# Kernel optimization log

Measured on AMD Instinct MI355X. Metric: run time of the kernel, lower is better.

Reference implementation:

```python
import jax, jax.numpy as jnp
import numpy as np

PATCH = 8
EPS = 1e-5


def _conv2d(x, w, b, groups=1, padding='VALID'):
    # x: NCHW, w: OIHW
    y = jax.lax.conv_general_dilated(
        x, w, window_strides=(1, 1), padding=padding,
        feature_group_count=groups,
        dimension_numbers=('NCHW', 'OIHW', 'NCHW'))
    return y + b[None, :, None, None]


def setup_inputs() -> dict:
    key = jax.random.key(0)
    ks = jax.random.split(key, 8)
    B, C, H, W = 4, 48, 256, 256
    C6, C2 = C * 6, C * 2
    x = jax.random.normal(ks[0], (B, C, H, W), dtype=jnp.float32)
    w_hidden = jax.random.normal(ks[1], (C6, C, 1, 1), dtype=jnp.float32) * 0.05
    b_hidden = jnp.zeros((C6,), dtype=jnp.float32)
    w_dw = jax.random.normal(ks[2], (C6, 1, 3, 3), dtype=jnp.float32) * 0.05
    b_dw = jnp.zeros((C6,), dtype=jnp.float32)
    gamma = jnp.ones((C2,), dtype=jnp.float32)
    beta = jnp.zeros((C2,), dtype=jnp.float32)
    w_out = jax.random.normal(ks[3], (C, C2, 1, 1), dtype=jnp.float32) * 0.05
    b_out = jnp.zeros((C,), dtype=jnp.float32)
    return {'x': x, 'w_hidden': w_hidden, 'b_hidden': b_hidden,
            'w_dw': w_dw, 'b_dw': b_dw, 'gamma': gamma, 'beta': beta,
            'w_out': w_out, 'b_out': b_out}


def reference(x, w_hidden, b_hidden, w_dw, b_dw, gamma, beta, w_out, b_out):
    B, C, H, W = x.shape
    C6 = 6 * C
    hidden = _conv2d(x, w_hidden, b_hidden)                       # [B,6C,H,W]
    qkv = _conv2d(hidden, w_dw, b_dw, groups=C6, padding='SAME')  # depthwise 3x3
    q, k, v = jnp.split(qkv, 3, axis=1)                           # each [B,2C,H,W]
    C2 = 2 * C
    hp, wp = H // PATCH, W // PATCH
    # same flat reshape as torch .reshape(b,c,h/p,w/p,p,p)
    q_patch = q.reshape(B, C2, hp, wp, PATCH, PATCH)
    k_patch = k.reshape(B, C2, hp, wp, PATCH, PATCH)
    q_fft = jnp.fft.rfft2(q_patch)                                # complex, last two axes
    k_fft = jnp.fft.rfft2(k_patch)
    out = jnp.fft.irfft2(q_fft * k_fft, s=(PATCH, PATCH))
    out = out.reshape(B, C2, H, W)
    # LayerNorm over channel dim (torch LayerNorm(2C) on [B,HW,2C])
    mu = jnp.mean(out, axis=1, keepdims=True)
    var = jnp.var(out, axis=1, keepdims=True)
    normed = (out - mu) / jnp.sqrt(var + EPS)
    normed = normed * gamma[None, :, None, None] + beta[None, :, None, None]
    return _conv2d(v * normed, w_out, b_out)                      # [B,C,H,W]
```

## Files before the change

### kernel.cpp

```cpp
#include <hip/hip_runtime.h>


#define B_ 4
#define C_ 48
#define H_ 256
#define W_ 256
#define ROWS 68
#define XT_STR 52
#define HID_STR 204
#define QK_STR 68
#define AV_STR 40

#define OFF_HID 0
#define OFF_QS  6528
#define OFF_KS  10880
#define OFF_OSH 15232
#define OFF_MU  27520
#define OFF_RS  27776
#define SMEM_BYTES 28032

typedef __attribute__((ext_vector_type(8))) short short8;
typedef __attribute__((ext_vector_type(4))) float floatx4;
union U128 { unsigned long long u[2]; short8 s; };

__device__ __forceinline__ float bf2f(unsigned short u) {
  return __uint_as_float(((unsigned int)u) << 16);
}
__device__ __forceinline__ unsigned short f2bf(float f) {
  unsigned int x = __float_as_uint(f);
  x += 0x7FFFu + ((x >> 16) & 1u);
  return (unsigned short)(x >> 16);
}
__device__ __forceinline__ unsigned long long pack4(float a, float b, float c, float d) {
  return (unsigned long long)f2bf(a) | ((unsigned long long)f2bf(b) << 16) |
         ((unsigned long long)f2bf(c) << 32) | ((unsigned long long)f2bf(d) << 48);
}

__global__ void fsas_prep(const float* __restrict__ wh, const float* __restrict__ wo,
                          unsigned short* __restrict__ ws) {
  int idx = blockIdx.x * 256 + threadIdx.x;
  if (idx < 12288) {
    int kk = idx & 63, t = idx >> 6;
    int m = t & 31, ch = t >> 5;
    float v = 0.f;
    if (kk < 48) {
      int c6 = (m < 16) ? (ch * 16 + m) : (96 + ch * 16 + (m - 16));
      v = wh[c6 * 48 + kk];
    }
    ws[idx] = f2bf(v);
  } else if (idx < 18432) {
    int e = idx - 12288;
    int kk = e & 63, t = e >> 6;
    int m = t & 15, ch = t >> 4;
    float v = (kk < 48) ? wh[(192 + ch * 16 + m) * 48 + kk] : 0.f;
    ws[idx] = f2bf(v);
  } else if (idx < 23040) {
    int e = idx - 18432;
    int kk = e & 31, t = e >> 5;
    int co = t % 48, pr = t / 48;
    ws[idx] = f2bf(wo[co * 96 + pr * 32 + kk]);
  }
}

__global__ __launch_bounds__(256, 4) void fsas_fused(
    const float* __restrict__ x,   const float* __restrict__ bh,
    const float* __restrict__ wdw, const float* __restrict__ bdw,
    const float* __restrict__ gam, const float* __restrict__ bet,
    const float* __restrict__ bo,  const unsigned short* __restrict__ ws,
    float* __restrict__ y)
{
  __shared__ __align__(16) char smem[SMEM_BYTES];
  unsigned short* xs_t = (unsigned short*)(smem);
  unsigned short* hid  = (unsigned short*)(smem + OFF_HID);
  float* qs = (float*)(smem + OFF_QS);
  float* ks = (float*)(smem + OFF_KS);
  unsigned short* osh = (unsigned short*)(smem + OFF_OSH);
  float* mu = (float*)(smem + OFF_MU);
  float* rs = (float*)(smem + OFF_RS);
  unsigned short* avp = (unsigned short*)(smem + OFF_QS);
  float2* part = (float2*)(smem + OFF_HID);

  const unsigned short* wqk = ws;
  const unsigned short* wv1 = ws + 12288;
  const unsigned short* w2p = ws + 18432;

  const int tid  = threadIdx.x;
  const int wseg = blockIdx.x;
  const int h    = blockIdx.y;
  const int b    = blockIdx.z;
  const int w0   = wseg * 64;
  const int lane = tid & 63;
  const int wv   = tid >> 6;
  const int ln   = lane & 15;
  const int quad = lane >> 4;
  const int pbase = wv * 16 + ln;

  for (int p = tid; p < 208; p += 256)
    *(unsigned long long*)(xs_t + p * XT_STR + 48) = 0ull;
  if (tid < 8) *(unsigned int*)(smem + 21632 + tid * 4) = 0u;
  for (int r = wv; r < 144; r += 4) {
    int c = r / 3, rr = r - c * 3;
    int gr = h - 1 + rr;
    bool rok = (gr >= 0) && (gr < H_);
    const float* xrow = x + (((b * C_) + c) * H_ + (rok ? gr : 0)) * W_;
    {
      int cc = lane, gc = w0 - 1 + cc;
      float v = 0.f;
      if (rok && gc >= 0 && gc < W_) v = xrow[gc];
      xs_t[(rr * ROWS + cc) * XT_STR + c] = f2bf(v);
    }
    if (lane < 4) {
      int cc = 64 + lane, gc = w0 - 1 + cc;
      float v = 0.f;
      if (cc < 66 && rok && gc < W_) v = xrow[gc];
      xs_t[(rr * ROWS + cc) * XT_STR + c] = f2bf(v);
    }
  }
  __syncthreads();

  short8 f00, f01, f10, f11, f20, f21, f30, f31;
  int pvm = 0;
  {
    U128 t0, t1;
    const unsigned short* bp0 = xs_t + (pbase)       * XT_STR + quad * 8;
    const unsigned short* bp1 = xs_t + (pbase + 64)  * XT_STR + quad * 8;
    const unsigned short* bp2 = xs_t + (pbase + 128) * XT_STR + quad * 8;
    t0.u[0] = *(const unsigned long long*)(bp0);
    t0.u[1] = *(const unsigned long long*)(bp0 + 4);
    t1.u[0] = *(const unsigned long long*)(bp0 + 32);
    t1.u[1] = *(const unsigned long long*)(bp0 + 36);
    asm("" : "=a"(f00) : "0"(t0.s));
    asm("" : "=a"(f01) : "0"(t1.s));
    t0.u[0] = *(const unsigned long long*)(bp1);
    t0.u[1] = *(const unsigned long long*)(bp1 + 4);
    t1.u[0] = *(const unsigned long long*)(bp1 + 32);
    t1.u[1] = *(const unsigned long long*)(bp1 + 36);
    asm("" : "=a"(f10) : "0"(t0.s));
    asm("" : "=a"(f11) : "0"(t1.s));
    t0.u[0] = *(const unsigned long long*)(bp2);
    t0.u[1] = *(const unsigned long long*)(bp2 + 4);
    t1.u[0] = *(const unsigned long long*)(bp2 + 32);
    t1.u[1] = *(const unsigned long long*)(bp2 + 36);
    asm("" : "=a"(f20) : "0"(t0.s));
    asm("" : "=a"(f21) : "0"(t1.s));
    t0.u[0] = 0ull; t0.u[1] = 0ull; t1.u[0] = 0ull; t1.u[1] = 0ull;
    if (wv == 0) {
      const unsigned short* bp3 = xs_t + (pbase + 192) * XT_STR + quad * 8;
      t0.u[0] = *(const unsigned long long*)(bp3);
      t0.u[1] = *(const unsigned long long*)(bp3 + 4);
      t1.u[0] = *(const unsigned long long*)(bp3 + 32);
      t1.u[1] = *(const unsigned long long*)(bp3 + 36);
    }
    asm("" : "=a"(f30) : "0"(t0.s));
    asm("" : "=a"(f31) : "0"(t1.s));
    #pragma unroll
    for (int i = 0; i < 4; ++i) {
      int p = pbase + i * 64;
      int rr = p / ROWS, cc = p - rr * ROWS;
      int gr = h - 1 + rr, gc = w0 - 1 + cc;
      bool pv = (rr < 3) && (cc < 66) && (gr >= 0) && (gr < H_) && (gc >= 0) && (gc < W_);
      pvm |= (pv ? 1 : 0) << i;
    }
  }
  __syncthreads();

  auto run_b1 = [&](const unsigned short* wA, int arow, int bhb) {
    short8 a0 = *(const short8*)(wA + ((arow + ln) * 64 + quad * 8));
    short8 a1 = *(const short8*)(wA + ((arow + ln) * 64 + 32 + quad * 8));
    floatx4 bb;
    #pragma unroll
    for (int r = 0; r < 4; ++r) bb[r] = bh[bhb + quad * 4 + r];
    unsigned short* hb = hid + (quad * 4) * HID_STR + pbase;
    {
      floatx4 acc = bb;
      acc = __builtin_amdgcn_mfma_f32_16x16x32_bf16(a0, f00, acc, 0, 0, 0);
      acc = __builtin_amdgcn_mfma_f32_16x16x32_bf16(a1, f01, acc, 0, 0, 0);
      bool pv = (pvm & 1) != 0;
      #pragma unroll
      for (int r = 0; r < 4; ++r) hb[r * HID_STR] = pv ? f2bf(acc[r]) : (unsigned short)0;
    }
    {
      floatx4 acc = bb;
      acc = __builtin_amdgcn_mfma_f32_16x16x32_bf16(a0, f10, acc, 0, 0, 0);
      acc = __builtin_amdgcn_mfma_f32_16x16x32_bf16(a1, f11, acc, 0, 0, 0);
      bool pv = (pvm & 2) != 0;
      #pragma unroll
      for (int r = 0; r < 4; ++r) hb[r * HID_STR + 64] = pv ? f2bf(acc[r]) : (unsigned short)0;
    }
    {
      floatx4 acc = bb;
      acc = __builtin_amdgcn_mfma_f32_16x16x32_bf16(a0, f20, acc, 0, 0, 0);
      acc = __builtin_amdgcn_mfma_f32_16x16x32_bf16(a1, f21, acc, 0, 0, 0);
      bool pv = (pvm & 4) != 0;
      #pragma unroll
      for (int r = 0; r < 4; ++r) hb[r * HID_STR + 128] = pv ? f2bf(acc[r]) : (unsigned short)0;
    }
    if (wv == 0) {
      floatx4 acc = bb;
      acc = __builtin_amdgcn_mfma_f32_16x16x32_bf16(a0, f30, acc, 0, 0, 0);
      acc = __builtin_amdgcn_mfma_f32_16x16x32_bf16(a1, f31, acc, 0, 0, 0);
      bool pv = (pvm & 8) != 0;
      if (ln < 12) {
        #pragma unroll
        for (int r = 0; r < 4; ++r) hb[r * HID_STR + 192] = pv ? f2bf(acc[r]) : (unsigned short)0;
      }
    }
  };
  auto run_b2 = [&](int c6base, float* dst) {
    int cl = tid >> 4, pg4 = tid & 15, p0 = pg4 * 4;
    int c6 = c6base + cl;
    const float* wd = wdw + c6 * 9;
    float bb = bdw[c6];
    float a4[4] = {bb, bb, bb, bb};
    #pragma unroll
    for (int di = 0; di < 3; ++di) {
      const unsigned short* hrow = hid + cl * HID_STR + di * ROWS + p0;
      unsigned long long lo = *(const unsigned long long*)(hrow);
      unsigned int ex = *(const unsigned int*)(hrow + 4);
      float hf[6];
      #pragma unroll
      for (int t = 0; t < 4; ++t) hf[t] = bf2f((unsigned short)(lo >> (16 * t)));
      hf[4] = bf2f((unsigned short)ex);
      hf[5] = bf2f((unsigned short)(ex >> 16));
      #pragma unroll
      for (int dj = 0; dj < 3; ++dj) {
        float w = wd[di * 3 + dj];
        #pragma unroll
        for (int t = 0; t < 4; ++t) a4[t] += w * hf[t + dj];
      }
    }
    *(float4*)(dst + cl * QK_STR + p0) = make_float4(a4[0], a4[1], a4[2], a4[3]);
  };
  auto run_b3 = [&](int c2base) {
    int cl = tid >> 4, r4 = tid & 15, uu = r4 >> 1, vh = r4 & 1;
    const float* qrow = qs + cl * QK_STR;
    const float* krow = ks + cl * QK_STR;
    float a4[4] = {0.f, 0.f, 0.f, 0.f};
    #pragma unroll
    for (int i = 0; i < 8; ++i) {
      float4 q0 = *(const float4*)(qrow + i * 8);
      float4 q1 = *(const float4*)(qrow + i * 8 + 4);
      int ri = (uu - i) & 7;
      float4 ka = *(const float4*)(krow + ri * 8 + vh * 4);
      float4 kb = *(const float4*)(krow + ri * 8 + (vh ^ 1) * 4);
      float qf[8] = {q0.x, q0.y, q0.z, q0.w, q1.x, q1.y, q1.z, q1.w};
      float kr[8] = {ka.x, ka.y, ka.z, ka.w, kb.x, kb.y, kb.z, kb.w};
      #pragma unroll
      for (int vvi = 0; vvi < 4; ++vvi)
        #pragma unroll
        for (int j = 0; j < 8; ++j)
          a4[vvi] += qf[j] * kr[(vvi - j) & 7];
    }
    int c2 = c2base + cl;
    *(unsigned long long*)(osh + c2 * 64 + uu * 8 + vh * 4) = pack4(a4[0], a4[1], a4[2], a4[3]);
  };

  #pragma unroll 1
  for (int chunk = 0; chunk < 6; ++chunk) {
    if (chunk > 0) run_b3((chunk - 1) * 16);
    __builtin_amdgcn_sched_barrier(0);
    run_b1(wqk, chunk * 32, chunk * 16);
    __syncthreads();
    run_b2(chunk * 16, qs);
    __syncthreads();
    run_b1(wqk, chunk * 32 + 16, 96 + chunk * 16);
    __syncthreads();
    run_b2(96 + chunk * 16, ks);
    __syncthreads();
  }
  run_b3(80);
  __syncthreads();

  {
    int p = tid & 63, seg = tid >> 6;
    float s = 0.f, s2 = 0.f;
    for (int c = seg * 24; c < seg * 24 + 24; ++c) {
      float ov = bf2f(osh[c * 64 + p]);
      s += ov; s2 += ov * ov;
    }
    part[seg * 64 + p] = make_float2(s, s2);
  }
  __syncthreads();
  if (tid < 64) {
    float s = 0.f, s2 = 0.f;
    #pragma unroll
    for (int seg = 0; seg < 4; ++seg) {
      float2 pr2 = part[seg * 64 + tid];
      s += pr2.x; s2 += pr2.y;
    }
    float m = s * (1.f / 96.f);
    float var = s2 * (1.f / 96.f) - m * m;
    mu[tid] = m;
    rs[tid] = rsqrtf(var + 1e-5f);
  }
  __syncthreads();

  floatx4 oacc[3];
  #pragma unroll
  for (int mt = 0; mt < 3; ++mt)
    #pragma unroll
    for (int r = 0; r < 4; ++r) oacc[mt][r] = bo[mt * 16 + quad * 4 + r];

  #pragma unroll 1
  for (int pr = 0; pr < 3; ++pr) {
    #pragma unroll 1
    for (int sub = 0; sub < 2; ++sub) {
      int chunk = pr * 2 + sub;
      run_b1(wv1, chunk * 16, 192 + chunk * 16);
      __syncthreads();
      {
        int lc = tid >> 4, pg4 = tid & 15, p0 = pg4 * 4;
        int c2 = chunk * 16 + lc, c6 = 192 + c2;
        const float* wd = wdw + c6 * 9;
        float bb = bdw[c6];
        float a4[4] = {bb, bb, bb, bb};
        #pragma unroll
        for (int di = 0; di < 3; ++di) {
          const unsigned short* hrow = hid + lc * HID_STR + di * ROWS + p0;
          unsigned long long lo = *(const unsigned long long*)(hrow);
          unsigned int ex = *(const unsigned int*)(hrow + 4);
          float hf[6];
          #pragma unroll
          for (int t = 0; t < 4; ++t) hf[t] = bf2f((unsigned short)(lo >> (16 * t)));
          hf[4] = bf2f((unsigned short)ex);
          hf[5] = bf2f((unsigned short)(ex >> 16));
          #pragma unroll
          for (int dj = 0; dj < 3; ++dj) {
            float w = wd[di * 3 + dj];
            #pragma unroll
            for (int t = 0; t < 4; ++t) a4[t] += w * hf[t + dj];
          }
        }
        float gv = gam[c2], bev = bet[c2];
        #pragma unroll
        for (int t = 0; t < 4; ++t) {
          int p = p0 + t;
          float o = bf2f(osh[c2 * 64 + p]);
          float a = ((o - mu[p]) * rs[p] * gv + bev) * a4[t];
          avp[p * AV_STR + sub * 16 + lc] = f2bf(a);
        }
      }
      __syncthreads();
    }
    __builtin_amdgcn_sched_barrier(0);
    {
      const unsigned short* bp = avp + (wv * 16 + ln) * AV_STR + quad * 8;
      U128 bfr;
      bfr.u[0] = *(const unsigned long long*)(bp);
      bfr.u[1] = *(const unsigned long long*)(bp + 4);
      #pragma unroll
      for (int mt = 0; mt < 3; ++mt) {
        short8 af = *(const short8*)(w2p + ((pr * 48 + mt * 16 + ln) * 32 + quad * 8));
        oacc[mt] = __builtin_amdgcn_mfma_f32_16x16x32_bf16(af, bfr.s, oacc[mt], 0, 0, 0);
      }
    }
  }

  #pragma unroll
  for (int mt = 0; mt < 3; ++mt)
    #pragma unroll
    for (int r = 0; r < 4; ++r) {
      int co = mt * 16 + quad * 4 + r;
      y[(((b * C_) + co) * H_ + h) * W_ + w0 + wv * 16 + ln] = oacc[mt][r];
    }
}

extern "C" void kernel_launch(void* const* d_in, const int* in_sizes, int n_in,
                              void* d_out, int out_size, void* d_ws, size_t ws_size,
                              hipStream_t stream) {
  const float* x   = (const float*)d_in[0];
  const float* wh  = (const float*)d_in[1];
  const float* bh  = (const float*)d_in[2];
  const float* wdw = (const float*)d_in[3];
  const float* bdw = (const float*)d_in[4];
  const float* g   = (const float*)d_in[5];
  const float* be  = (const float*)d_in[6];
  const float* wo  = (const float*)d_in[7];
  const float* bo  = (const float*)d_in[8];
  float* y = (float*)d_out;
  unsigned short* ws = (unsigned short*)d_ws;

  fsas_prep<<<dim3(90), 256, 0, stream>>>(wh, wo, ws);
  dim3 grid(4, H_, B_);
  fsas_fused<<<grid, 256, 0, stream>>>(x, bh, wdw, bdw, g, be, bo, ws, y);
}
```

Measured before the change: 376.1 us.

## Double-buffer hidden and q tiles to halve barriers in qk chunk loop

Splits the hidden-activation scratch into two buffers and q into two ping-pong buffers. Each chunk can then compute the next 1x1 conv stage while running the previous depthwise and FFT-convolution stages, with two barriers per chunk instead of four. This raises shared memory from about 28KB to 39KB per block, which may reduce occupancy under launch_bounds(256,4). AV_STR also shrinks from 40 to 36.

```diff
diff --git a/kernel.cpp b/kernel.cpp
--- a/kernel.cpp
+++ b/kernel.cpp
@@ -9,15 +9,17 @@
 #define XT_STR 52
 #define HID_STR 204
 #define QK_STR 68
-#define AV_STR 40
-
-#define OFF_HID 0
-#define OFF_QS  6528
-#define OFF_KS  10880
-#define OFF_OSH 15232
-#define OFF_MU  27520
-#define OFF_RS  27776
-#define SMEM_BYTES 28032
+#define AV_STR 36
+
+#define OFF_H1  0
+#define OFF_H2  6528
+#define OFF_QSA 13056
+#define OFF_QSB 17408
+#define OFF_KS  21760
+#define OFF_OSH 26112
+#define OFF_MU  38400
+#define OFF_RS  38656
+#define SMEM_BYTES 38912
 
 typedef __attribute__((ext_vector_type(8))) short short8;
 typedef __attribute__((ext_vector_type(4))) float floatx4;
@@ -71,14 +73,16 @@
 {
   __shared__ __align__(16) char smem[SMEM_BYTES];
   unsigned short* xs_t = (unsigned short*)(smem);
-  unsigned short* hid  = (unsigned short*)(smem + OFF_HID);
-  float* qs = (float*)(smem + OFF_QS);
-  float* ks = (float*)(smem + OFF_KS);
+  unsigned short* h1  = (unsigned short*)(smem + OFF_H1);
+  unsigned short* h2  = (unsigned short*)(smem + OFF_H2);
+  float* qsA = (float*)(smem + OFF_QSA);
+  float* qsB = (float*)(smem + OFF_QSB);
+  float* ks  = (float*)(smem + OFF_KS);
   unsigned short* osh = (unsigned short*)(smem + OFF_OSH);
   float* mu = (float*)(smem + OFF_MU);
   float* rs = (float*)(smem + OFF_RS);
-  unsigned short* avp = (unsigned short*)(smem + OFF_QS);
-  float2* part = (float2*)(smem + OFF_HID);
+  unsigned short* avp = (unsigned short*)(smem + OFF_QSA);
+  float2* part = (float2*)(smem + OFF_H1);
 
   const unsigned short* wqk = ws;
   const unsigned short* wv1 = ws + 12288;
@@ -164,13 +168,13 @@
   }
   __syncthreads();
 
-  auto run_b1 = [&](const unsigned short* wA, int arow, int bhb) {
+  auto run_b1 = [&](const unsigned short* wA, int arow, int bhb, unsigned short* hbuf) {
     short8 a0 = *(const short8*)(wA + ((arow + ln) * 64 + quad * 8));
     short8 a1 = *(const short8*)(wA + ((arow + ln) * 64 + 32 + quad * 8));
     floatx4 bb;
     #pragma unroll
     for (int r = 0; r < 4; ++r) bb[r] = bh[bhb + quad * 4 + r];
-    unsigned short* hb = hid + (quad * 4) * HID_STR + pbase;
+    unsigned short* hb = hbuf + (quad * 4) * HID_STR + pbase;
     {
       floatx4 acc = bb;
       acc = __builtin_amdgcn_mfma_f32_16x16x32_bf16(a0, f00, acc, 0, 0, 0);
@@ -206,7 +210,7 @@
       }
     }
   };
-  auto run_b2 = [&](int c6base, float* dst) {
+  auto run_b2 = [&](int c6base, float* dst, const unsigned short* hsrc) {
     int cl = tid >> 4, pg4 = tid & 15, p0 = pg4 * 4;
     int c6 = c6base + cl;
     const float* wd = wdw + c6 * 9;
@@ -214,7 +218,7 @@
     float a4[4] = {bb, bb, bb, bb};
     #pragma unroll
     for (int di = 0; di < 3; ++di) {
-      const unsigned short* hrow = hid + cl * HID_STR + di * ROWS + p0;
+      const unsigned short* hrow = hsrc + cl * HID_STR + di * ROWS + p0;
       unsigned long long lo = *(const unsigned long long*)(hrow);
       unsigned int ex = *(const unsigned int*)(hrow + 4);
       float hf[6];
@@ -231,9 +235,9 @@
     }
     *(float4*)(dst + cl * QK_STR + p0) = make_float4(a4[0], a4[1], a4[2], a4[3]);
   };
-  auto run_b3 = [&](int c2base) {
+  auto run_b3 = [&](int c2base, const float* qsrc) {
     int cl = tid >> 4, r4 = tid & 15, uu = r4 >> 1, vh = r4 & 1;
-    const float* qrow = qs + cl * QK_STR;
+    const float* qrow = qsrc + cl * QK_STR;
     const float* krow = ks + cl * QK_STR;
     float a4[4] = {0.f, 0.f, 0.f, 0.f};
     #pragma unroll
@@ -257,18 +261,18 @@
 
   #pragma unroll 1
   for (int chunk = 0; chunk < 6; ++chunk) {
-    if (chunk > 0) run_b3((chunk - 1) * 16);
+    run_b1(wqk, chunk * 32, chunk * 16, h1);
+    if (chunk > 0) run_b2(96 + (chunk - 1) * 16, ks, h2);
+    __syncthreads();
+    if (chunk > 0) run_b3((chunk - 1) * 16, (chunk & 1) ? qsA : qsB);
     __builtin_amdgcn_sched_barrier(0);
-    run_b1(wqk, chunk * 32, chunk * 16);
+    run_b1(wqk, chunk * 32 + 16, 96 + chunk * 16, h2);
+    run_b2(chunk * 16, (chunk & 1) ? qsB : qsA, h1);
     __syncthreads();
-    run_b2(chunk * 16, qs);
-    __syncthreads();
-    run_b1(wqk, chunk * 32 + 16, 96 + chunk * 16);
-    __syncthreads();
-    run_b2(96 + chunk * 16, ks);
-    __syncthreads();
-  }
-  run_b3(80);
+  }
+  run_b2(96 + 80, ks, h2);
+  __syncthreads();
+  run_b3(80, qsB);
   __syncthreads();
 
   {
@@ -306,7 +310,7 @@
     #pragma unroll 1
     for (int sub = 0; sub < 2; ++sub) {
       int chunk = pr * 2 + sub;
-      run_b1(wv1, chunk * 16, 192 + chunk * 16);
+      run_b1(wv1, chunk * 16, 192 + chunk * 16, h1);
       __syncthreads();
       {
         int lc = tid >> 4, pg4 = tid & 15, p0 = pg4 * 4;
@@ -316,7 +320,7 @@
         float a4[4] = {bb, bb, bb, bb};
         #pragma unroll
         for (int di = 0; di < 3; ++di) {
-          const unsigned short* hrow = hid + lc * HID_STR + di * ROWS + p0;
+          const unsigned short* hrow = h1 + lc * HID_STR + di * ROWS + p0;
           unsigned long long lo = *(const unsigned long long*)(hrow);
           unsigned int ex = *(const unsigned int*)(hrow + 4);
           float hf[6];
```

Result: no change. 381.9 us (+1.5%).
